# Kernel optimization log

Hardware: AMD Instinct MI355X
Metric: run time of the kernel (lower is better)

## Reference

```python
import jax, jax.numpy as jnp
import numpy as np

N_NODES = 50000
N_EDGES = 1600000
IN_DIM = 128
HEADS = 8
OUT_C = 16  # per-head channels; HEADS*OUT_C == IN_DIM -> residual active
NEG_SLOPE = 0.2
BN_EPS = 1e-5


def setup_inputs() -> dict:
    key = jax.random.key(0)
    ks = jax.random.split(key, 8)
    x = jax.random.normal(ks[0], (N_NODES, IN_DIM), dtype=jnp.float32)
    edge_index = jax.random.randint(ks[1], (2, N_EDGES), 0, N_NODES, dtype=jnp.int64)
    # GATConv params (PyG: shared lin for src/dst on single-tensor input)
    W = jax.random.normal(ks[2], (IN_DIM, HEADS * OUT_C), dtype=jnp.float32) / np.sqrt(IN_DIM)
    att_src = jax.random.normal(ks[3], (HEADS, OUT_C), dtype=jnp.float32) / np.sqrt(OUT_C)
    att_dst = jax.random.normal(ks[4], (HEADS, OUT_C), dtype=jnp.float32) / np.sqrt(OUT_C)
    bias = jnp.zeros((HEADS * OUT_C,), dtype=jnp.float32)
    # BatchNorm1d affine params
    gamma = jnp.ones((HEADS * OUT_C,), dtype=jnp.float32)
    beta = jnp.zeros((HEADS * OUT_C,), dtype=jnp.float32)
    return {"x": x, "edge_index": edge_index, "W": W, "att_src": att_src,
            "att_dst": att_dst, "bias": bias, "gamma": gamma, "beta": beta}


def reference(x, edge_index, W, att_src, att_dst, bias, gamma, beta):
    N = x.shape[0]
    H, C = att_src.shape
    src, dst = edge_index[0], edge_index[1]

    xl = (x @ W).reshape(N, H, C)                      # [N,H,C]
    a_src = jnp.sum(xl * att_src[None], axis=-1)       # [N,H]
    a_dst = jnp.sum(xl * att_dst[None], axis=-1)       # [N,H]

    e = jax.nn.leaky_relu(a_src[src] + a_dst[dst], NEG_SLOPE)  # [E,H]
    # segment softmax over incoming edges of each dst node
    m = jax.ops.segment_max(e, dst, num_segments=N)    # [N,H], -inf for empty
    m = jnp.where(jnp.isfinite(m), m, 0.0)
    ex = jnp.exp(e - m[dst])                           # [E,H]
    denom = jax.ops.segment_sum(ex, dst, num_segments=N)
    alpha = ex / (denom[dst] + 1e-16)                  # [E,H]

    out = jax.ops.segment_sum(alpha[:, :, None] * xl[src], dst, num_segments=N)  # [N,H,C]
    h = out.reshape(N, H * C) + bias

    # BatchNorm1d (training mode: batch statistics, biased variance)
    mean = jnp.mean(h, axis=0)
    var = jnp.mean((h - mean) ** 2, axis=0)
    h = (h - mean) * jax.lax.rsqrt(var + BN_EPS) * gamma + beta

    h = jax.nn.relu(h)
    return x + h  # residual (in_dim == H*C)
```

## Files before the change

### kernel.cpp

```cpp
#include <hip/hip_runtime.h>
#include <hip/hip_fp16.h>
#include <math.h>

#define N_NODES 50000
#define N_EDGES 1600000
#define DIM 128
#define HEADS 8
#define NEG_SLOPE 0.2f
#define BN_EPS 1e-5f

typedef _Float16 f16x8 __attribute__((ext_vector_type(8)));
typedef float f32x4 __attribute__((ext_vector_type(4)));

#define NBUCK 196
#define SEGCAP 12288
#define CHUNK 8192
#define NB_A ((N_EDGES + CHUNK - 1) / CHUNK)
#define LIN_NB ((N_NODES + 127) / 128)
#define FUSED_NB (NB_A + LIN_NB)

struct BinAShm {
    int hist[NBUCK], excl[NBUCK], gbase[NBUCK], cnt2[NBUCK];
    int sc[256];
    unsigned int buf[CHUNK];
};
struct LinShm { __half wh[16384]; };

__global__ __launch_bounds__(512) void k_linbinA(
        const float* __restrict__ x, const float* __restrict__ W,
        const float* __restrict__ att_s, const float* __restrict__ att_d,
        const int* __restrict__ ei, int* __restrict__ bcur,
        unsigned int* __restrict__ pairs, __half* __restrict__ xlh,
        float* __restrict__ a_src, float* __restrict__ a_dst) {
    __shared__ union { BinAShm a; LinShm l; } sh;
    const int t = threadIdx.x;

    if (blockIdx.x < NB_A) {
        const int base = blockIdx.x * CHUNK;
        const int cnt = min(CHUNK, N_EDGES - base);

        for (int j = t; j < NBUCK; j += 512) { sh.a.hist[j] = 0; sh.a.cnt2[j] = 0; }
        __syncthreads();
        for (int i = t * 4; i < cnt; i += 2048) {
            const int4 dv = *(const int4*)(ei + N_EDGES + base + i);
            atomicAdd(&sh.a.hist[dv.x >> 8], 1);
            atomicAdd(&sh.a.hist[dv.y >> 8], 1);
            atomicAdd(&sh.a.hist[dv.z >> 8], 1);
            atomicAdd(&sh.a.hist[dv.w >> 8], 1);
        }
        __syncthreads();
        if (t < 256) sh.a.sc[t] = (t < NBUCK) ? sh.a.hist[t] : 0;
        __syncthreads();
        for (int d = 1; d < 256; d <<= 1) {
            int xo = 0;
            if (t < 256 && t >= d) xo = sh.a.sc[t - d];
            __syncthreads();
            if (t < 256) sh.a.sc[t] += xo;
            __syncthreads();
        }
        if (t < NBUCK) {
            sh.a.excl[t] = sh.a.sc[t] - sh.a.hist[t];
            sh.a.gbase[t] = t * SEGCAP + atomicAdd(&bcur[t], sh.a.hist[t]);
        }
        __syncthreads();
        for (int i = t * 4; i < cnt; i += 2048) {
            const int4 sv = *(const int4*)(ei + base + i);
            const int4 dv = *(const int4*)(ei + N_EDGES + base + i);
            const int ss[4] = {sv.x, sv.y, sv.z, sv.w};
            const int dd[4] = {dv.x, dv.y, dv.z, dv.w};
            #pragma unroll
            for (int k = 0; k < 4; ++k) {
                const int b = dd[k] >> 8;
                const int r = atomicAdd(&sh.a.cnt2[b], 1);
                sh.a.buf[sh.a.excl[b] + r] = (unsigned int)ss[k]
                    | ((unsigned int)(dd[k] & 255) << 16) | ((unsigned int)b << 24);
            }
        }
        __syncthreads();
        for (int i = t; i < cnt; i += 512) {
            const unsigned int u = sh.a.buf[i];
            const int b = u >> 24;
            pairs[sh.a.gbase[b] + (i - sh.a.excl[b])] = u & 0xFFFFFF;
        }
    } else {
        for (int v = t; v < 2048; v += 512) {
            const int g = v >> 6, lane = v & 63;
            const int nt = g >> 2, kt = g & 3;
            const int q = lane >> 4, n = lane & 15;
            #pragma unroll
            for (int j = 0; j < 8; ++j)
                sh.l.wh[(size_t)(g * 64 + lane) * 8 + j] =
                    __float2half(W[(kt * 32 + q * 8 + j) * DIM + nt * 16 + n]);
        }
        __syncthreads();

        const int wave = t >> 6;
        const int lane = t & 63;
        const int q = lane >> 4, n = lane & 15;
        const int nb = ((blockIdx.x - NB_A) * 8 + wave) * 16;

        const int rowA = min(nb + n, N_NODES - 1);
        const float* xr = x + (size_t)rowA * DIM;
        f16x8 a[4];
        #pragma unroll
        for (int kt = 0; kt < 4; ++kt) {
            const float4 p0 = *(const float4*)(xr + kt * 32 + q * 8);
            const float4 p1 = *(const float4*)(xr + kt * 32 + q * 8 + 4);
            a[kt][0] = (_Float16)p0.x; a[kt][1] = (_Float16)p0.y;
            a[kt][2] = (_Float16)p0.z; a[kt][3] = (_Float16)p0.w;
            a[kt][4] = (_Float16)p1.x; a[kt][5] = (_Float16)p1.y;
            a[kt][6] = (_Float16)p1.z; a[kt][7] = (_Float16)p1.w;
        }

        f32x4 acc[8];
        #pragma unroll
        for (int nt = 0; nt < 8; ++nt) acc[nt] = (f32x4){0.f, 0.f, 0.f, 0.f};

        const f16x8* wb = (const f16x8*)sh.l.wh;
        #pragma unroll
        for (int nt = 0; nt < 8; ++nt) {
            #pragma unroll
            for (int kt = 0; kt < 4; ++kt) {
                const f16x8 b = wb[(nt * 4 + kt) * 64 + lane];
                acc[nt] = __builtin_amdgcn_mfma_f32_16x16x32_f16(a[kt], b, acc[nt], 0, 0, 0);
            }
        }

        const int r0 = nb + q * 4;
        #pragma unroll
        for (int nt = 0; nt < 8; ++nt) {
            const float as = att_s[nt * 16 + n];
            const float ad = att_d[nt * 16 + n];
            #pragma unroll
            for (int r = 0; r < 4; ++r) {
                const int row = r0 + r;
                const float v = acc[nt][r];
                float s = v * as;
                float d = v * ad;
                #pragma unroll
                for (int off = 8; off; off >>= 1) {
                    s += __shfl_xor(s, off, 16);
                    d += __shfl_xor(d, off, 16);
                }
                if (row < N_NODES) {
                    xlh[(size_t)row * DIM + nt * 16 + n] = __float2half(v);
                    if (n == 0) {
                        a_src[row * HEADS + nt] = s;
                        a_dst[row * HEADS + nt] = d;
                    }
                }
            }
        }
    }
}

__global__ __launch_bounds__(1024) void k_binB(const unsigned int* __restrict__ pairs,
                                               const int* __restrict__ bcur,
                                               unsigned short* __restrict__ csr,
                                               int2* __restrict__ nrange,
                                               float* __restrict__ gsums) {
    __shared__ int hist[256], eh[256], excl[256], cnt2[256];
    __shared__ int plen;
    __shared__ unsigned short out[SEGCAP];
    const int t = threadIdx.x;
    const int b = blockIdx.x;
    if (b == 0 && t < 256) gsums[t] = 0.f;
    const int lo = b * SEGCAP;
    const int cnt = bcur[b];

    if (t < 256) { hist[t] = 0; cnt2[t] = 0; }
    __syncthreads();
    for (int i = t; i < cnt; i += 1024)
        atomicAdd(&hist[pairs[lo + i] >> 16], 1);
    __syncthreads();
    if (t < 256) { eh[t] = (hist[t] + 1) & ~1; excl[t] = eh[t]; }
    __syncthreads();
    for (int d = 1; d < 256; d <<= 1) {
        int xo = 0;
        if (t < 256 && t >= d) xo = excl[t - d];
        __syncthreads();
        if (t < 256) excl[t] += xo;
        __syncthreads();
    }
    if (t < 256) excl[t] -= eh[t];
    if (t == 255) plen = excl[255] + eh[255];
    __syncthreads();
    for (int i = t; i < cnt; i += 1024) {
        const unsigned int u = pairs[lo + i];
        const int dl = u >> 16;
        const int r = atomicAdd(&cnt2[dl], 1);
        out[excl[dl] + r] = (unsigned short)(u & 0xFFFF);
    }
    __syncthreads();
    const int pl = plen;
    for (int i = t; i < pl; i += 1024)
        csr[2 * lo + i] = out[i];
    if (t < 256) {
        const int node = (b << 8) + t;
        if (node < N_NODES) {
            int2 rg;
            rg.x = 2 * lo + excl[t];
            rg.y = rg.x + hist[t];
            nrange[node] = rg;
        }
    }
}

#define AGG_NB (N_NODES / 4)

__global__ void k_aggr6(const int2* __restrict__ nrange,
                        const unsigned short* __restrict__ csr,
                        const float* __restrict__ a_src, const float* __restrict__ a_dst,
                        const __half* __restrict__ xlh, float* __restrict__ y) {
    const int d = blockIdx.x * 4 + (threadIdx.x >> 6);
    const int lane = threadIdx.x & 63;
    const int c2 = lane << 1;
    const int h = lane >> 3;
    const int2 rg = nrange[d];
    const int lo = rg.x, hi = rg.y;
    const float ad = a_dst[d * HEADS + h];
    float acc0 = 0.f, acc1 = 0.f, dsum = 0.f;
    int i = lo;
    for (; i + 8 <= hi; i += 8) {
        int s[8];
        float e[8];
        __half2 xv[8];
        #pragma unroll
        for (int j = 0; j < 8; ++j) s[j] = csr[i + j];
        #pragma unroll
        for (int j = 0; j < 8; ++j) e[j] = a_src[s[j] * HEADS + h] + ad;
        #pragma unroll
        for (int j = 0; j < 8; ++j)
            xv[j] = *(const __half2*)(xlh + (size_t)s[j] * DIM + c2);
        #pragma unroll
        for (int j = 0; j < 8; ++j) {
            const float w = __expf(fmaxf(e[j], NEG_SLOPE * e[j]));
            const float2 f = __half22float2(xv[j]);
            acc0 = fmaf(w, f.x, acc0);
            acc1 = fmaf(w, f.y, acc1);
            dsum += w;
        }
    }
    for (; i < hi; ++i) {
        const int s = csr[i];
        const float e = a_src[s * HEADS + h] + ad;
        const __half2 xv = *(const __half2*)(xlh + (size_t)s * DIM + c2);
        const float w = __expf(fmaxf(e, NEG_SLOPE * e));
        const float2 f = __half22float2(xv);
        acc0 = fmaf(w, f.x, acc0); acc1 = fmaf(w, f.y, acc1); dsum += w;
    }
    const float inv = 1.f / (dsum + 1e-16f);
    float2 o; o.x = acc0 * inv; o.y = acc1 * inv;
    *(float2*)(y + (size_t)d * DIM + c2) = o;
}

__global__ void k_stats(const float* __restrict__ y, const float* __restrict__ bias,
                        float* __restrict__ gsums) {
    const int c = threadIdx.x;
    const float b = bias[c];
    float s = 0.f, ss = 0.f;
    for (int n = blockIdx.x; n < N_NODES; n += gridDim.x) {
        const float h = y[n * DIM + c] + b;
        s += h;
        ss += h * h;
    }
    atomicAdd(&gsums[c], s);
    atomicAdd(&gsums[DIM + c], ss);
}

__global__ void k_final(float* __restrict__ y, const float* __restrict__ x,
                        const float* __restrict__ sums, const float* __restrict__ sumsq,
                        const float* __restrict__ gamma, const float* __restrict__ beta,
                        const float* __restrict__ bias) {
    const int q = blockIdx.x * blockDim.x + threadIdx.x;
    const int cq = q & (DIM / 4 - 1);
    const float4 sm = ((const float4*)sums)[cq];
    const float4 sq = ((const float4*)sumsq)[cq];
    const float4 gm = ((const float4*)gamma)[cq];
    const float4 bt = ((const float4*)beta)[cq];
    const float4 bs = ((const float4*)bias)[cq];
    float4 v = ((const float4*)y)[q];
    const float4 xv = ((const float4*)x)[q];
    const float inv_n = 1.f / (float)N_NODES;
#define BNC(c) { const float mean = sm.c * inv_n;                         \
                 const float var = sq.c * inv_n - mean * mean;            \
                 const float sc = rsqrtf(var + BN_EPS) * gm.c;            \
                 const float sh = bt.c + (bs.c - mean) * sc;              \
                 v.c = xv.c + fmaxf(v.c * sc + sh, 0.f); }
    BNC(x) BNC(y) BNC(z) BNC(w)
#undef BNC
    ((float4*)y)[q] = v;
}

extern "C" void kernel_launch(void* const* d_in, const int* in_sizes, int n_in,
                              void* d_out, int out_size, void* d_ws, size_t ws_size,
                              hipStream_t stream) {
    const float* x     = (const float*)d_in[0];
    const int*   ei    = (const int*)  d_in[1];
    const float* W     = (const float*)d_in[2];
    const float* att_s = (const float*)d_in[3];
    const float* att_d = (const float*)d_in[4];
    const float* bias  = (const float*)d_in[5];
    const float* gamma = (const float*)d_in[6];
    const float* beta  = (const float*)d_in[7];
    float* y = (float*)d_out;

    __half* xlh  = (__half*)d_ws;
    float* a_src = (float*)(xlh + (size_t)N_NODES * DIM);
    float* a_dst = a_src + (size_t)N_NODES * HEADS;
    float* sums  = a_dst + (size_t)N_NODES * HEADS;
    float* sumsq = sums  + DIM;
    int*   bcur  = (int*)(sumsq + DIM);
    int2*  nrange = (int2*)(bcur + 256);
    unsigned int* pairs = (unsigned int*)(nrange + N_NODES);
    unsigned short* csr = (unsigned short*)pairs;

    hipMemsetAsync(bcur, 0, 256 * sizeof(int), stream);
    k_linbinA<<<FUSED_NB, 512, 0, stream>>>(x, W, att_s, att_d, ei, bcur, pairs,
                                            xlh, a_src, a_dst);
    k_binB<<<NBUCK, 1024, 0, stream>>>(pairs, bcur, csr, nrange, sums);
    k_aggr6<<<AGG_NB, 256, 0, stream>>>(nrange, csr, a_src, a_dst, xlh, y);
    k_stats<<<512, DIM, 0, stream>>>(y, bias, sums);
    k_final<<<(size_t)N_NODES * DIM / 4 / 256, 256, 0, stream>>>(y, x, sums, sumsq,
                                                                 gamma, beta, bias);
}
```

Baseline: 234.2 us.

## Gather whole rows with 16-byte loads across four edge groups per wavefront

The aggregation kernel is restructured so each wavefront splits into four 16-lane groups. Each group handles a different edge and loads 8 fp16 channels per lane with one 16-byte load, replacing per-lane 4-byte half2 gathers. Partial sums are then combined across groups with cross-lane shuffles. The attention logits are pre-scaled by log2(e) in the linear kernel so that exp2f can replace __expf; this is valid because leaky ReLU is positively homogeneous. The cost is more accumulator registers and a shuffle reduction per node.

```diff
diff --git a/kernel.cpp b/kernel.cpp
--- a/kernel.cpp
+++ b/kernel.cpp
@@ -145,8 +145,8 @@
                 if (row < N_NODES) {
                     xlh[(size_t)row * DIM + nt * 16 + n] = __float2half(v);
                     if (n == 0) {
-                        a_src[row * HEADS + nt] = s;
-                        a_dst[row * HEADS + nt] = d;
+                        a_src[row * HEADS + nt] = s * 1.44269504f;
+                        a_dst[row * HEADS + nt] = d * 1.44269504f;
                     }
                 }
             }
@@ -208,50 +208,65 @@
 
 #define AGG_NB (N_NODES / 4)
 
-__global__ void k_aggr6(const int2* __restrict__ nrange,
+__global__ void k_aggr7(const int2* __restrict__ nrange,
                         const unsigned short* __restrict__ csr,
                         const float* __restrict__ a_src, const float* __restrict__ a_dst,
                         const __half* __restrict__ xlh, float* __restrict__ y) {
     const int d = blockIdx.x * 4 + (threadIdx.x >> 6);
     const int lane = threadIdx.x & 63;
-    const int c2 = lane << 1;
-    const int h = lane >> 3;
+    const int g = lane >> 4;
+    const int cl = lane & 15;
+    const int h = cl >> 1;
     const int2 rg = nrange[d];
     const int lo = rg.x, hi = rg.y;
     const float ad = a_dst[d * HEADS + h];
-    float acc0 = 0.f, acc1 = 0.f, dsum = 0.f;
+
+    float acc[8];
+    #pragma unroll
+    for (int k = 0; k < 8; ++k) acc[k] = 0.f;
+    float dsum = 0.f;
+
     int i = lo;
     for (; i + 8 <= hi; i += 8) {
-        int s[8];
-        float e[8];
-        __half2 xv[8];
-        #pragma unroll
-        for (int j = 0; j < 8; ++j) s[j] = csr[i + j];
-        #pragma unroll
-        for (int j = 0; j < 8; ++j) e[j] = a_src[s[j] * HEADS + h] + ad;
-        #pragma unroll
-        for (int j = 0; j < 8; ++j)
-            xv[j] = *(const __half2*)(xlh + (size_t)s[j] * DIM + c2);
-        #pragma unroll
-        for (int j = 0; j < 8; ++j) {
-            const float w = __expf(fmaxf(e[j], NEG_SLOPE * e[j]));
-            const float2 f = __half22float2(xv[j]);
-            acc0 = fmaf(w, f.x, acc0);
-            acc1 = fmaf(w, f.y, acc1);
-            dsum += w;
-        }
-    }
-    for (; i < hi; ++i) {
-        const int s = csr[i];
-        const float e = a_src[s * HEADS + h] + ad;
-        const __half2 xv = *(const __half2*)(xlh + (size_t)s * DIM + c2);
-        const float w = __expf(fmaxf(e, NEG_SLOPE * e));
-        const float2 f = __half22float2(xv);
-        acc0 = fmaf(w, f.x, acc0); acc1 = fmaf(w, f.y, acc1); dsum += w;
-    }
+        const int s0 = csr[i + g];
+        const int s1 = csr[i + 4 + g];
+        const float as0 = a_src[s0 * HEADS + h];
+        const float as1 = a_src[s1 * HEADS + h];
+        const f16x8 x0 = *(const f16x8*)(xlh + (size_t)s0 * DIM + cl * 8);
+        const f16x8 x1 = *(const f16x8*)(xlh + (size_t)s1 * DIM + cl * 8);
+        const float e0 = as0 + ad;
+        const float e1 = as1 + ad;
+        const float w0 = exp2f(fmaxf(e0, NEG_SLOPE * e0));
+        const float w1 = exp2f(fmaxf(e1, NEG_SLOPE * e1));
+        dsum += w0 + w1;
+        #pragma unroll
+        for (int k = 0; k < 8; ++k) acc[k] = fmaf(w0, (float)x0[k], acc[k]);
+        #pragma unroll
+        for (int k = 0; k < 8; ++k) acc[k] = fmaf(w1, (float)x1[k], acc[k]);
+    }
+    for (; i < hi; i += 4) {
+        const int idx = i + g;
+        const int sv = csr[min(idx, hi - 1)];
+        const float e = a_src[sv * HEADS + h] + ad;
+        const f16x8 xv = *(const f16x8*)(xlh + (size_t)sv * DIM + cl * 8);
+        float w = exp2f(fmaxf(e, NEG_SLOPE * e));
+        if (idx >= hi) w = 0.f;
+        dsum += w;
+        #pragma unroll
+        for (int k = 0; k < 8; ++k) acc[k] = fmaf(w, (float)xv[k], acc[k]);
+    }
+    #pragma unroll
+    for (int k = 0; k < 8; ++k) {
+        acc[k] += __shfl_xor(acc[k], 16);
+        acc[k] += __shfl_xor(acc[k], 32);
+    }
+    dsum += __shfl_xor(dsum, 16);
+    dsum += __shfl_xor(dsum, 32);
     const float inv = 1.f / (dsum + 1e-16f);
-    float2 o; o.x = acc0 * inv; o.y = acc1 * inv;
-    *(float2*)(y + (size_t)d * DIM + c2) = o;
+    float2 o;
+    o.x = acc[2 * g] * inv;
+    o.y = acc[2 * g + 1] * inv;
+    *(float2*)(y + (size_t)d * DIM + cl * 8 + g * 2) = o;
 }
 
 __global__ void k_stats(const float* __restrict__ y, const float* __restrict__ bias,
@@ -319,7 +334,7 @@
     k_linbinA<<<FUSED_NB, 512, 0, stream>>>(x, W, att_s, att_d, ei, bcur, pairs,
                                             xlh, a_src, a_dst);
     k_binB<<<NBUCK, 1024, 0, stream>>>(pairs, bcur, csr, nrange, sums);
-    k_aggr6<<<AGG_NB, 256, 0, stream>>>(nrange, csr, a_src, a_dst, xlh, y);
+    k_aggr7<<<AGG_NB, 256, 0, stream>>>(nrange, csr, a_src, a_dst, xlh, y);
     k_stats<<<512, DIM, 0, stream>>>(y, bias, sums);
     k_final<<<(size_t)N_NODES * DIM / 4 / 256, 256, 0, stream>>>(y, x, sums, sumsq,
                                                                  gamma, beta, bias);
```

Result: no change. 230.7 us (-1.5%).
